# Optimization experiments

Hardware: AMD Instinct MI355X
Metric: run time of the kernel (lower is better)

Reference implementation:

```python
import jax, jax.numpy as jnp
import numpy as np

B, S, DIM = 4, 1024, 4096
HQ, HKV, HD = 32, 8, 128
MAX_SEQ = 2048
START_POS = 1024
THETA = 10000.0


def _rope_tables(start, seqlen, head_dim, theta):
    inv = 1.0 / (theta ** (np.arange(0, head_dim, 2, dtype=np.float32) / head_dim))
    pos = np.arange(start, start + seqlen, dtype=np.float32)
    ang = np.outer(pos, inv)  # [S, HD/2]
    return jnp.asarray(np.cos(ang)), jnp.asarray(np.sin(ang))


def setup_inputs() -> dict:
    key = jax.random.key(0)
    ks = jax.random.split(key, 8)
    sc = 1.0 / np.sqrt(DIM)
    x = jax.random.normal(ks[0], (B, S, DIM), jnp.float32)
    wq = jax.random.normal(ks[1], (DIM, HQ * HD), jnp.float32) * sc
    wk = jax.random.normal(ks[2], (DIM, HKV * HD), jnp.float32) * sc
    wv = jax.random.normal(ks[3], (DIM, HKV * HD), jnp.float32) * sc
    wo = jax.random.normal(ks[4], (HQ * HD, DIM), jnp.float32) * sc
    cache_k = jax.random.normal(ks[5], (B, MAX_SEQ, HKV, HD), jnp.float32)
    cache_v = jax.random.normal(ks[6], (B, MAX_SEQ, HKV, HD), jnp.float32)
    cos, sin = _rope_tables(START_POS, S, HD, THETA)
    return {"x": x, "wq": wq, "wk": wk, "wv": wv, "wo": wo,
            "freqs_cos": cos, "freqs_sin": sin,
            "cache_k": cache_k, "cache_v": cache_v, "start_pos": START_POS}


def _apply_rope(t, cos, sin):
    # t: [B, S, H, HD]; cos/sin: [S, HD/2]
    b, s, h, d = t.shape
    tr = t.reshape(b, s, h, d // 2, 2)
    xr, xi = tr[..., 0], tr[..., 1]
    c = cos[None, :, None, :]
    sn = sin[None, :, None, :]
    outr = xr * c - xi * sn
    outi = xr * sn + xi * c
    return jnp.stack([outr, outi], axis=-1).reshape(b, s, h, d)


def reference(x, wq, wk, wv, wo, freqs_cos, freqs_sin, cache_k, cache_v, start_pos):
    b, s, _ = x.shape
    rep = HQ // HKV
    q = (x @ wq).reshape(b, s, HQ, HD)
    k = (x @ wk).reshape(b, s, HKV, HD)
    v = (x @ wv).reshape(b, s, HKV, HD)
    q = _apply_rope(q, freqs_cos, freqs_sin)
    k = _apply_rope(k, freqs_cos, freqs_sin)
    # write new K/V into the cache at start_pos (static int -> static slice)
    cache_k = cache_k.at[:, start_pos:start_pos + s].set(k)
    cache_v = cache_v.at[:, start_pos:start_pos + s].set(v)
    keys = cache_k[:, : start_pos + s]     # [B, KV, HKV, HD]
    values = cache_v[:, : start_pos + s]
    # GQA: group query heads with their KV head instead of materializing repeat_kv
    qg = q.reshape(b, s, HKV, rep, HD)
    scores = jnp.einsum('bqhrd,bkhd->bhrqk', qg, keys) / jnp.sqrt(
        jnp.asarray(HD, x.dtype))
    probs = jax.nn.softmax(scores, axis=-1).astype(x.dtype)
    out = jnp.einsum('bhrqk,bkhd->bqhrd', probs, values)
    out = out.reshape(b, s, HQ * HD)
    return out @ wo
```

## Files before the change

### kernel.cpp

```cpp
#include <hip/hip_runtime.h>

typedef _Float16 half_t;
typedef _Float16 half8 __attribute__((ext_vector_type(8)));
typedef _Float16 half4v __attribute__((ext_vector_type(4)));
typedef _Float16 half2v __attribute__((ext_vector_type(2)));
typedef float floatx4 __attribute__((ext_vector_type(4)));

#define TOK 4096
#define DIM 4096
#define S_LEN 1024
#define B_SZ 4
#define HQ_N 32
#define HKV_N 8
#define HD_N 128
#define L_KV 2048
#define NKV 1024
#define NKV2 2048
#define QK_SCALE 0.08838834764831845f
#define LOG2E 1.4426950408889634f

__device__ __forceinline__ void gload_lds16(const void* g, void* l) {
  __builtin_amdgcn_global_load_lds(
      (const __attribute__((address_space(1))) unsigned int*)g,
      (__attribute__((address_space(3))) unsigned int*)l, 16, 0, 0);
}

__device__ __forceinline__ float max3f(float a, float b, float c) {
  return fmaxf(fmaxf(a, b), c);
}

__global__ __launch_bounds__(256) void prep_kernel(const float* __restrict__ x,
                                                   const float* __restrict__ wq,
                                                   const float* __restrict__ wk,
                                                   const float* __restrict__ wv,
                                                   const float* __restrict__ wo,
                                                   half_t* __restrict__ xh,
                                                   half_t* __restrict__ wqT,
                                                   half_t* __restrict__ kvT,
                                                   half_t* __restrict__ woT) {
  __shared__ half_t T[64 * 65];
  const int bid = blockIdx.x;
  const int tid = threadIdx.x;
  if (bid >= 10240) {
    int t = (bid - 10240) * 256 + tid;
    floatx4 v = *((const floatx4*)x + t);
    half4v o;
    o[0] = (half_t)v[0]; o[1] = (half_t)v[1]; o[2] = (half_t)v[2]; o[3] = (half_t)v[3];
    *((half4v*)xh + t) = o;
    return;
  }
  const float* in; half_t* out; int N; int lb;
  if (bid < 4096)      { in = wq; out = wqT; N = 4096; lb = bid; }
  else if (bid < 5120) { in = wk; out = kvT; N = 1024; lb = bid - 4096; }
  else if (bid < 6144) { in = wv; out = kvT + (size_t)NKV * DIM; N = 1024; lb = bid - 5120; }
  else                 { in = wo; out = woT; N = 4096; lb = bid - 6144; }
  const int nbx = N >> 6;
  const int n0 = (lb % nbx) * 64, k0 = (lb / nbx) * 64;
  #pragma unroll
  for (int i = 0; i < 16; ++i) {
    int idx = i * 256 + tid;
    int r = idx >> 6, c = idx & 63;
    T[c * 65 + r] = (half_t)in[(size_t)(k0 + r) * N + n0 + c];
  }
  __syncthreads();
  #pragma unroll
  for (int i = 0; i < 16; ++i) {
    int idx = i * 256 + tid;
    int rn = idx >> 6, ck = idx & 63;
    out[(size_t)(n0 + rn) * DIM + k0 + ck] = T[rn * 65 + ck];
  }
}

template <typename OT>
__global__ __launch_bounds__(256) void gemm_f16(const half_t* __restrict__ A,
                                                const half_t* __restrict__ BT,
                                                OT* __restrict__ C,
                                                int M, int N, int K) {
  __shared__ half_t As[128 * 32];
  __shared__ half_t Bs[128 * 32];
  const int tid = threadIdx.x;
  const int lane = tid & 63;
  const int w = tid >> 6;
  const int wr = w >> 1, wc = w & 1;
  const int g = lane >> 4, qr = lane & 15;
  const int m0 = blockIdx.y * 128, n0 = blockIdx.x * 128;
  floatx4 acc[4][4] = {};
  const int chb0 = tid & 192;
  for (int k0 = 0; k0 < K; k0 += 32) {
    #pragma unroll
    for (int i = 0; i < 2; ++i) {
      int chb = chb0 + 256 * i;
      int ch = chb + lane;
      int row = ch >> 2, c8 = ch & 3;
      gload_lds16(A + (size_t)(m0 + row) * K + k0 + c8 * 8, (char*)As + chb * 16);
      gload_lds16(BT + (size_t)(n0 + row) * K + k0 + c8 * 8, (char*)Bs + chb * 16);
    }
    __syncthreads();
    half8 af[4], bf[4];
    const int koff = g * 8;
    #pragma unroll
    for (int m = 0; m < 4; ++m)
      af[m] = *(const half8*)&As[(wr * 64 + m * 16 + qr) * 32 + koff];
    #pragma unroll
    for (int n = 0; n < 4; ++n)
      bf[n] = *(const half8*)&Bs[(wc * 64 + n * 16 + qr) * 32 + koff];
    #pragma unroll
    for (int m = 0; m < 4; ++m)
      #pragma unroll
      for (int n = 0; n < 4; ++n)
        acc[m][n] = __builtin_amdgcn_mfma_f32_16x16x32_f16(af[m], bf[n], acc[m][n], 0, 0, 0);
    __syncthreads();
  }
  #pragma unroll
  for (int m = 0; m < 4; ++m) {
    int rb = m0 + wr * 64 + m * 16 + g * 4;
    #pragma unroll
    for (int n = 0; n < 4; ++n) {
      int col = n0 + wc * 64 + n * 16 + qr;
      #pragma unroll
      for (int r = 0; r < 4; ++r)
        C[(size_t)(rb + r) * N + col] = (OT)acc[m][n][r];
    }
  }
}

template <typename OT, bool ROPE>
__global__ __launch_bounds__(512) void gemm256(const half_t* __restrict__ A,
                                               const half_t* __restrict__ BT,
                                               OT* __restrict__ C,
                                               const float* __restrict__ fc,
                                               const float* __restrict__ fs,
                                               half_t* __restrict__ qh,
                                               int M, int N, int K) {
  __shared__ __align__(16) char smem[131072];
  const int tid = threadIdx.x;
  const int lane = tid & 63, w = tid >> 6;
  const int g = lane >> 4, qr = lane & 15;
  const int wm = w >> 2, wn = w & 3;
  const int nbx = N >> 8;
  const int nwg = gridDim.x;
  const int cpx = nwg >> 3;
  const int bid = ((int)blockIdx.x & 7) * cpx + ((int)blockIdx.x >> 3);
  const int bx = bid % nbx, by = bid / nbx;
  const int m0 = by << 8, n0 = bx << 8;
  const int NT = K >> 6;

  const int ch0 = tid, ch1 = tid + 512;
  const int sr0 = ch0 >> 3, sc0 = (ch0 & 7) ^ (sr0 & 7);
  const int sr1 = ch1 >> 3, sc1 = (ch1 & 7) ^ (sr1 & 7);
  const size_t so0 = (size_t)sr0 * K + sc0 * 8;
  const size_t so1 = (size_t)sr1 * K + sc1 * 8;
  const int wb = (w * 64) * 16;
  const half_t* Ab = A + (size_t)m0 * K;
  const half_t* Bb = BT + (size_t)n0 * K;

#define G_STAGE(gsrc, ldst)                                   \
  do {                                                        \
    gload_lds16((gsrc) + so0, (char*)(ldst) + wb);            \
    gload_lds16((gsrc) + so1, (char*)(ldst) + wb + 8192);     \
  } while (0)

#define FRAG(base, row, kb) \
  (*(const half8*)((base) + ((((row) * 128) + (kb)) ^ (((row) & 7) << 4))))

  G_STAGE(Ab, smem);
  G_STAGE(Ab + (size_t)128 * K, smem + 16384);
  G_STAGE(Bb, smem + 65536);
  G_STAGE(Bb + (size_t)128 * K, smem + 81920);
  G_STAGE(Ab + 64, smem + 32768);
  G_STAGE(Bb + 64, smem + 98304);
  asm volatile("s_waitcnt vmcnt(4)" ::: "memory");
  __builtin_amdgcn_s_barrier();

  floatx4 acc[8][4] = {};
  half8 aF[4][2], bF0[2][2], bF1[2][2];

#define MFMA_Q(mh, nh, BF)                                                     \
  do {                                                                         \
    __builtin_amdgcn_s_setprio(1);                                             \
    _Pragma("unroll") for (int mf = 0; mf < 4; ++mf)                           \
    _Pragma("unroll") for (int nf = 0; nf < 2; ++nf)                           \
    _Pragma("unroll") for (int kk = 0; kk < 2; ++kk)                           \
      acc[(mh)*4 + mf][(nh)*2 + nf] = __builtin_amdgcn_mfma_f32_16x16x32_f16(  \
          aF[mf][kk], BF[nf][kk], acc[(mh)*4 + mf][(nh)*2 + nf], 0, 0, 0);     \
    __builtin_amdgcn_s_setprio(0);                                             \
  } while (0)

  for (int t = 0; t < NT; ++t) {
    const char* Ac = smem + ((t & 1) ? 32768 : 0);
    const char* Bc = smem + 65536 + ((t & 1) ? 32768 : 0);
    char* An = smem + ((t & 1) ? 0 : 32768);
    char* Bn = smem + 65536 + ((t & 1) ? 0 : 32768);
    const int t1 = (t + 1 < NT) ? t + 1 : NT - 1;
    const int t2 = (t + 2 < NT) ? t + 2 : NT - 1;
    #pragma unroll
    for (int mf = 0; mf < 4; ++mf)
      #pragma unroll
      for (int kk = 0; kk < 2; ++kk)
        aF[mf][kk] = FRAG(Ac, wm * 128 + mf * 16 + qr, kk * 64 + g * 16);
    #pragma unroll
    for (int nf = 0; nf < 2; ++nf)
      #pragma unroll
      for (int kk = 0; kk < 2; ++kk)
        bF0[nf][kk] = FRAG(Bc, wn * 64 + nf * 16 + qr, kk * 64 + g * 16);
    G_STAGE(Ab + (size_t)128 * K + t1 * 64, An + 16384);
    __builtin_amdgcn_s_barrier();
    asm volatile("s_waitcnt lgkmcnt(0)" ::: "memory");
    MFMA_Q(0, 0, bF0);
    __builtin_amdgcn_s_barrier();
    #pragma unroll
    for (int nf = 0; nf < 2; ++nf)
      #pragma unroll
      for (int kk = 0; kk < 2; ++kk)
        bF1[nf][kk] = FRAG(Bc, wn * 64 + 32 + nf * 16 + qr, kk * 64 + g * 16);
    G_STAGE(Bb + (size_t)128 * K + t1 * 64, Bn + 16384);
    __builtin_amdgcn_s_barrier();
    asm volatile("s_waitcnt lgkmcnt(0)" ::: "memory");
    MFMA_Q(0, 1, bF1);
    __builtin_amdgcn_s_barrier();
    #pragma unroll
    for (int mf = 0; mf < 4; ++mf)
      #pragma unroll
      for (int kk = 0; kk < 2; ++kk)
        aF[mf][kk] = FRAG(Ac, wm * 128 + 64 + mf * 16 + qr, kk * 64 + g * 16);
    __builtin_amdgcn_s_barrier();
    asm volatile("s_waitcnt lgkmcnt(0)" ::: "memory");
    MFMA_Q(1, 1, bF1);
    __builtin_amdgcn_s_barrier();
    G_STAGE(Ab + (size_t)t2 * 64, (char*)Ac);
    G_STAGE(Bb + (size_t)t2 * 64, (char*)Bc);
    __builtin_amdgcn_s_barrier();
    MFMA_Q(1, 0, bF0);
    asm volatile("s_waitcnt vmcnt(4)" ::: "memory");
    __builtin_amdgcn_s_barrier();
  }
  #pragma unroll
  for (int mh = 0; mh < 2; ++mh)
    #pragma unroll
    for (int mf = 0; mf < 4; ++mf) {
      const int rb = m0 + wm * 128 + mh * 64 + mf * 16 + g * 4;
      #pragma unroll
      for (int nh = 0; nh < 2; ++nh)
        #pragma unroll
        for (int nf = 0; nf < 2; ++nf) {
          const int col = n0 + wn * 64 + nh * 32 + nf * 16 + qr;
          floatx4 v = acc[mh * 4 + mf][nh * 2 + nf];
          if constexpr (ROPE) {
            const float QS2 = QK_SCALE * LOG2E;
            const int d = col & 127, hqh = col >> 7, j = d >> 1;
            #pragma unroll
            for (int r = 0; r < 4; ++r) {
              float pv = __shfl_xor(v[r], 1, 64);
              const int tokr = rb + r;
              const int s = tokr & 1023, bb = tokr >> 10;
              float c = fc[s * 64 + j], sn = fs[s * 64 + j];
              float outv = (qr & 1) ? (v[r] * c + pv * sn) : (v[r] * c - pv * sn);
              qh[(((size_t)(bb * HQ_N + hqh)) * S_LEN + s) * HD_N + d] =
                  (half_t)(outv * QS2);
            }
          } else {
            #pragma unroll
            for (int r = 0; r < 4; ++r)
              C[(size_t)(rb + r) * N + col] = (OT)v[r];
          }
        }
    }
#undef G_STAGE
#undef FRAG
#undef MFMA_Q
}

__global__ __launch_bounds__(256) void pack_k_kernel(const half_t* __restrict__ kvf,
                                                     const float* __restrict__ cache_k,
                                                     const float* __restrict__ cosT,
                                                     const float* __restrict__ sinT,
                                                     half_t* __restrict__ kh) {
  int t = blockIdx.x * 256 + threadIdx.x;
  int j = t & 63;
  int h = (t >> 6) & 7;
  int pos = (t >> 9) & 2047;
  int b = t >> 20;
  float xr, xi;
  if (pos < 1024) {
    const float* src = cache_k + ((size_t)(b * L_KV + pos) * HKV_N + h) * HD_N + 2 * j;
    xr = src[0]; xi = src[1];
  } else {
    int s = pos - 1024;
    const half_t* src = kvf + (size_t)(b * S_LEN + s) * NKV2 + h * HD_N + 2 * j;
    float r0 = (float)src[0], i0 = (float)src[1];
    float c = cosT[s * 64 + j], sn = sinT[s * 64 + j];
    xr = r0 * c - i0 * sn;
    xi = r0 * sn + i0 * c;
  }
  half2v o; o[0] = (half_t)xr; o[1] = (half_t)xi;
  *(half2v*)(kh + ((size_t)(b * HKV_N + h) * L_KV + pos) * HD_N + 2 * j) = o;
}

__global__ __launch_bounds__(256) void pack_vt_kernel(const half_t* __restrict__ kvf,
                                                      const float* __restrict__ cache_v,
                                                      half_t* __restrict__ vt) {
  __shared__ half_t T[128 * 129];
  const int tid = threadIdx.x;
  const int blk = blockIdx.x;
  const int pt = blk & 15;
  const int h = (blk >> 4) & 7;
  const int b = blk >> 7;
  const int p0 = pt * 128;
  #pragma unroll
  for (int i = 0; i < 64; ++i) {
    int idx = i * 256 + tid;
    int p = idx >> 7, d = idx & 127;
    int pos = p0 + p;
    float v;
    if (pos < 1024)
      v = cache_v[((size_t)(b * L_KV + pos) * HKV_N + h) * HD_N + d];
    else
      v = (float)kvf[(size_t)(b * S_LEN + (pos - 1024)) * NKV2 + NKV + h * HD_N + d];
    T[d * 129 + p] = (half_t)v;
  }
  __syncthreads();
  #pragma unroll
  for (int i = 0; i < 64; ++i) {
    int idx = i * 256 + tid;
    int d = idx >> 7, p = idx & 127;
    vt[((size_t)(b * HKV_N + h) * HD_N + d) * L_KV + p0 + p] = T[d * 129 + p];
  }
}

__global__ __launch_bounds__(256, 2) void attn_kernel(const half_t* __restrict__ qh,
                                                      const half_t* __restrict__ kh,
                                                      const half_t* __restrict__ vt,
                                                      half_t* __restrict__ ah) {
  __shared__ __align__(16) char smem[73728];
  const int tid = threadIdx.x;
  const int lane = tid & 63, w = tid >> 6;
  const int g = lane >> 4, qr = lane & 15;
  const int hq = blockIdx.x, qt = blockIdx.y, b = blockIdx.z;
  const int hkv = hq >> 2;
  const half_t* qbase =
      qh + ((size_t)((b * HQ_N + hq) * S_LEN) + qt * 128 + w * 16 + qr) * HD_N;
  half8 qfA[4], qfB[4];
  #pragma unroll
  for (int c = 0; c < 4; ++c) {
    qfA[c] = *(const half8*)(qbase + g * 8 + c * 32);
    qfB[c] = *(const half8*)(qbase + (size_t)64 * HD_N + g * 8 + c * 32);
  }
  floatx4 accA[8] = {}, accB[8] = {};
  float mA = -1e30f, lA = 0.f, mB = -1e30f, lB = 0.f;
  const half_t* kg = kh + (size_t)(b * HKV_N + hkv) * L_KV * HD_N;
  const half_t* vg = vt + (size_t)(b * HKV_N + hkv) * HD_N * L_KV;

  const int sw = (qr & 7) << 4;
  const char* kqkP[4];
  #pragma unroll
  for (int c = 0; c < 4; ++c) kqkP[c] = smem + qr * 256 + ((g * 16 + c * 64) ^ sw);
  const char* vP[2];
  #pragma unroll
  for (int kc = 0; kc < 2; ++kc)
    vP[kc] = smem + 32768 + qr * 128 + ((kc * 64 + g * 16) ^ sw);
  char* pB = smem + 65536 + w * 2048 + qr * 128;
  char* pwQ[4];
  #pragma unroll
  for (int ts = 0; ts < 4; ++ts) pwQ[ts] = pB + ((ts * 32 + g * 8) ^ sw);
  const char* prR[2];
  #pragma unroll
  for (int kc = 0; kc < 2; ++kc) prR[kc] = pB + ((kc * 64 + g * 16) ^ sw);

  const int r0 = tid >> 4;
  const int c8k = (tid & 15) ^ (r0 & 7);
  const half_t* kp[4];
  #pragma unroll
  for (int j = 0; j < 4; ++j) kp[j] = kg + (size_t)(r0 + 16 * j) * HD_N + c8k * 8;
  const int d0v = tid >> 3;
  const int p8v = (tid & 7) ^ (d0v & 7);
  const half_t* vp[4];
  #pragma unroll
  for (int j = 0; j < 4; ++j) vp[j] = vg + (size_t)(d0v + 32 * j) * L_KV + p8v * 8;
  const int ldsb = (tid & 192) * 16;

#define ISSUE_STAGE(NKB)                                                     \
  do {                                                                       \
    _Pragma("unroll") for (int j2 = 0; j2 < 4; ++j2)                         \
      gload_lds16(kp[j2], smem + (NKB) + ldsb + j2 * 4096);                  \
    _Pragma("unroll") for (int j2 = 0; j2 < 4; ++j2)                         \
      gload_lds16(vp[j2], smem + 32768 + (NKB) + ldsb + j2 * 4096);          \
    _Pragma("unroll") for (int j2 = 0; j2 < 4; ++j2) {                       \
      kp[j2] += 8192; vp[j2] += 64;                                          \
    }                                                                        \
  } while (0)

#define QKT2(KB)                                                               \
  do {                                                                         \
    __builtin_amdgcn_s_setprio(1);                                             \
    _Pragma("unroll") for (int ts = 0; ts < 4; ++ts) {                         \
      floatx4 tqA = {0.f, 0.f, 0.f, 0.f}, tqB = {0.f, 0.f, 0.f, 0.f};          \
      _Pragma("unroll") for (int c = 0; c < 4; ++c) {                          \
        half8 kfr = *(const half8*)(kqkP[c] + (KB) + ts * 4096);               \
        tqA = __builtin_amdgcn_mfma_f32_16x16x32_f16(kfr, qfA[c], tqA, 0,0,0); \
        tqB = __builtin_amdgcn_mfma_f32_16x16x32_f16(kfr, qfB[c], tqB, 0,0,0); \
      }                                                                        \
      scA[ts*4+0]=tqA[0]; scA[ts*4+1]=tqA[1];                                  \
      scA[ts*4+2]=tqA[2]; scA[ts*4+3]=tqA[3];                                  \
      scB[ts*4+0]=tqB[0]; scB[ts*4+1]=tqB[1];                                  \
      scB[ts*4+2]=tqB[2]; scB[ts*4+3]=tqB[3];                                  \
    }                                                                          \
    __builtin_amdgcn_s_setprio(0);                                             \
  } while (0)

#define SOFTMAX(SC, ACC, MR, LR, PF)                                           \
  do {                                                                         \
    float pmax = fmaxf(                                                        \
        max3f(max3f(SC[0], SC[1], SC[2]), max3f(SC[3], SC[4], SC[5]),          \
              max3f(SC[6], SC[7], SC[8])),                                     \
        max3f(max3f(SC[9], SC[10], SC[11]), max3f(SC[12], SC[13], SC[14]),     \
              SC[15]));                                                        \
    pmax = fmaxf(pmax, __shfl_xor(pmax, 16, 64));                              \
    pmax = fmaxf(pmax, __shfl_xor(pmax, 32, 64));                              \
    const bool skip = __all(pmax - MR <= 8.f);                                 \
    const float mnew = skip ? MR : fmaxf(MR, pmax);                            \
    float rs = 0.f;                                                            \
    _Pragma("unroll") for (int j = 0; j < 16; ++j) {                           \
      float p;                                                                 \
      asm("v_exp_f32 %0, %1" : "=v"(p) : "v"(SC[j] - mnew));                   \
      SC[j] = p; rs += p;                                                      \
    }                                                                          \
    rs += __shfl_xor(rs, 16, 64);                                              \
    rs += __shfl_xor(rs, 32, 64);                                              \
    if (skip) {                                                                \
      LR += rs;                                                                \
    } else {                                                                   \
      float scl;                                                               \
      asm("v_exp_f32 %0, %1" : "=v"(scl) : "v"(MR - mnew));                    \
      LR = LR * scl + rs;                                                      \
      float f0 = __shfl(scl, g * 4 + 0, 64), f1 = __shfl(scl, g * 4 + 1, 64);  \
      float f2 = __shfl(scl, g * 4 + 2, 64), f3 = __shfl(scl, g * 4 + 3, 64);  \
      _Pragma("unroll") for (int n = 0; n < 8; ++n) {                          \
        ACC[n][0] *= f0; ACC[n][1] *= f1; ACC[n][2] *= f2; ACC[n][3] *= f3;    \
      }                                                                        \
      MR = mnew;                                                               \
    }                                                                          \
    _Pragma("unroll") for (int ts = 0; ts < 4; ++ts) {                         \
      half2v lo = __builtin_bit_cast(                                          \
          half2v, __builtin_amdgcn_cvt_pkrtz(SC[ts * 4 + 0], SC[ts * 4 + 1])); \
      half2v hi = __builtin_bit_cast(                                          \
          half2v, __builtin_amdgcn_cvt_pkrtz(SC[ts * 4 + 2], SC[ts * 4 + 3])); \
      *(half4v*)(pwQ[ts]) = __builtin_shufflevector(lo, hi, 0, 1, 2, 3);       \
    }                                                                          \
    PF[0] = *(const half8*)(prR[0]);                                           \
    PF[1] = *(const half8*)(prR[1]);                                           \
  } while (0)

#define PV2(KB)                                                                \
  do {                                                                         \
    __builtin_amdgcn_s_setprio(1);                                             \
    _Pragma("unroll") for (int kc = 0; kc < 2; ++kc)                           \
      _Pragma("unroll") for (int n = 0; n < 8; ++n) {                          \
        half8 vfr = *(const half8*)(vP[kc] + (KB) + n * 2048);                 \
        accA[n] = __builtin_amdgcn_mfma_f32_16x16x32_f16(pfA[kc], vfr,         \
                                                         accA[n], 0, 0, 0);   \
        accB[n] = __builtin_amdgcn_mfma_f32_16x16x32_f16(pfB[kc], vfr,         \
                                                         accB[n], 0, 0, 0);   \
      }                                                                        \
    __builtin_amdgcn_s_setprio(0);                                             \
  } while (0)

#define COMPUTE2(KB)                          \
  do {                                        \
    float scA[16], scB[16];                   \
    half8 pfA[2], pfB[2];                     \
    QKT2(KB);                                 \
    SOFTMAX(scA, accA, mA, lA, pfA);          \
    SOFTMAX(scB, accB, mB, lB, pfB);          \
    PV2(KB);                                  \
  } while (0)

#define ENDBAR                                          \
  do {                                                  \
    asm volatile("s_waitcnt vmcnt(0)" ::: "memory");    \
    __builtin_amdgcn_s_barrier();                       \
  } while (0)

  ISSUE_STAGE(0);
  ENDBAR;
  for (int it = 0; it < 15; ++it) {
    ISSUE_STAGE(16384); COMPUTE2(0);     ENDBAR;
    ISSUE_STAGE(0);     COMPUTE2(16384); ENDBAR;
  }
  ISSUE_STAGE(16384); COMPUTE2(0); ENDBAR;
  COMPUTE2(16384);

#define WRITE_OUT(ACC, LR, SOFF)                                            \
  do {                                                                      \
    float il0 = 1.f / __shfl(LR, g * 4 + 0, 64);                            \
    float il1 = 1.f / __shfl(LR, g * 4 + 1, 64);                            \
    float il2 = 1.f / __shfl(LR, g * 4 + 2, 64);                            \
    float il3 = 1.f / __shfl(LR, g * 4 + 3, 64);                            \
    const int tokb = b * S_LEN + qt * 128 + (SOFF) + w * 16 + g * 4;        \
    _Pragma("unroll") for (int n = 0; n < 8; ++n) {                         \
      const int col = hq * HD_N + n * 16 + qr;                              \
      ah[(size_t)(tokb + 0) * DIM + col] = (half_t)(ACC[n][0] * il0);       \
      ah[(size_t)(tokb + 1) * DIM + col] = (half_t)(ACC[n][1] * il1);       \
      ah[(size_t)(tokb + 2) * DIM + col] = (half_t)(ACC[n][2] * il2);       \
      ah[(size_t)(tokb + 3) * DIM + col] = (half_t)(ACC[n][3] * il3);       \
    }                                                                       \
  } while (0)

  WRITE_OUT(accA, lA, 0);
  WRITE_OUT(accB, lB, 64);
#undef ISSUE_STAGE
#undef QKT2
#undef SOFTMAX
#undef PV2
#undef COMPUTE2
#undef ENDBAR
#undef WRITE_OUT
}

extern "C" void kernel_launch(void* const* d_in, const int* in_sizes, int n_in,
                              void* d_out, int out_size, void* d_ws, size_t ws_size,
                              hipStream_t stream) {
  (void)in_sizes; (void)n_in; (void)out_size; (void)ws_size;
  const float* x = (const float*)d_in[0];
  const float* wq = (const float*)d_in[1];
  const float* wk = (const float*)d_in[2];
  const float* wv = (const float*)d_in[3];
  const float* wo = (const float*)d_in[4];
  const float* fc = (const float*)d_in[5];
  const float* fs = (const float*)d_in[6];
  const float* ck = (const float*)d_in[7];
  const float* cv = (const float*)d_in[8];

  char* ws = (char*)d_ws;
  size_t off = 0;
  auto alloc = [&](size_t bytes) {
    char* p = ws + off;
    off += (bytes + 255) & ~(size_t)255;
    return p;
  };
  half_t* xh    = (half_t*)alloc((size_t)TOK * DIM * 2);
  half_t* wqT   = (half_t*)alloc((size_t)DIM * DIM * 2);
  half_t* kvT   = (half_t*)alloc((size_t)NKV2 * DIM * 2);
  half_t* woT   = (half_t*)alloc((size_t)DIM * DIM * 2);
  half_t* qh    = (half_t*)alloc((size_t)B_SZ * HQ_N * S_LEN * HD_N * 2);
  half_t* kvf16 = (half_t*)alloc((size_t)TOK * NKV2 * 2);
  half_t* kh    = (half_t*)alloc((size_t)B_SZ * HKV_N * L_KV * HD_N * 2);
  half_t* vth   = (half_t*)alloc((size_t)B_SZ * HKV_N * HD_N * L_KV * 2);
  half_t* ah    = wqT;

  prep_kernel<<<dim3(26624), dim3(256), 0, stream>>>(x, wq, wk, wv, wo, xh, wqT, kvT, woT);
  gemm256<half_t, true><<<dim3((TOK / 256) * (DIM / 256)), dim3(512), 0, stream>>>(
      xh, wqT, (half_t*)nullptr, fc, fs, qh, TOK, DIM, DIM);
  gemm_f16<half_t><<<dim3(NKV2 / 128, TOK / 128), dim3(256), 0, stream>>>(xh, kvT, kvf16, TOK, NKV2, DIM);
  pack_k_kernel<<<dim3(B_SZ * L_KV * HKV_N * 64 / 256), dim3(256), 0, stream>>>(kvf16, ck, fc, fs, kh);
  pack_vt_kernel<<<dim3(B_SZ * HKV_N * (L_KV / 128)), dim3(256), 0, stream>>>(kvf16, cv, vth);
  attn_kernel<<<dim3(HQ_N, S_LEN / 128, B_SZ), dim3(256), 0, stream>>>(qh, kh, vth, ah);
  gemm256<float, false><<<dim3((TOK / 256) * (DIM / 256)), dim3(512), 0, stream>>>(
      ah, woT, (float*)d_out, nullptr, nullptr, nullptr, TOK, DIM, DIM);
}
```

Measured before the change: 626.4 us.

## Single-buffer K/V tiles in attention to fit four blocks per CU

Replaces the double-buffered K/V LDS staging with single K and V buffers and interleaves their loads with the softmax and PV phases, cutting shared memory from 72KB to 40KB. Launch bounds rise to four blocks per CU so that more waves hide latency. In exchange each iteration has more barriers, prefetch distance is shorter, and the tighter register budget may cause spills.

```diff
diff --git a/kernel.cpp b/kernel.cpp
--- a/kernel.cpp
+++ b/kernel.cpp
@@ -327,11 +327,11 @@
   }
 }
 
-__global__ __launch_bounds__(256, 2) void attn_kernel(const half_t* __restrict__ qh,
+__global__ __launch_bounds__(256, 4) void attn_kernel(const half_t* __restrict__ qh,
                                                       const half_t* __restrict__ kh,
                                                       const half_t* __restrict__ vt,
                                                       half_t* __restrict__ ah) {
-  __shared__ __align__(16) char smem[73728];
+  __shared__ __align__(16) char smem[40960];
   const int tid = threadIdx.x;
   const int lane = tid & 63, w = tid >> 6;
   const int g = lane >> 4, qr = lane & 15;
@@ -357,8 +357,8 @@
   const char* vP[2];
   #pragma unroll
   for (int kc = 0; kc < 2; ++kc)
-    vP[kc] = smem + 32768 + qr * 128 + ((kc * 64 + g * 16) ^ sw);
-  char* pB = smem + 65536 + w * 2048 + qr * 128;
+    vP[kc] = smem + 16384 + qr * 128 + ((kc * 64 + g * 16) ^ sw);
+  char* pB = smem + 32768 + w * 2048 + qr * 128;
   char* pwQ[4];
   #pragma unroll
   for (int ts = 0; ts < 4; ++ts) pwQ[ts] = pB + ((ts * 32 + g * 8) ^ sw);
@@ -378,24 +378,29 @@
   for (int j = 0; j < 4; ++j) vp[j] = vg + (size_t)(d0v + 32 * j) * L_KV + p8v * 8;
   const int ldsb = (tid & 192) * 16;
 
-#define ISSUE_STAGE(NKB)                                                     \
+#define STAGE_K                                                              \
   do {                                                                       \
-    _Pragma("unroll") for (int j2 = 0; j2 < 4; ++j2)                         \
-      gload_lds16(kp[j2], smem + (NKB) + ldsb + j2 * 4096);                  \
-    _Pragma("unroll") for (int j2 = 0; j2 < 4; ++j2)                         \
-      gload_lds16(vp[j2], smem + 32768 + (NKB) + ldsb + j2 * 4096);          \
     _Pragma("unroll") for (int j2 = 0; j2 < 4; ++j2) {                       \
-      kp[j2] += 8192; vp[j2] += 64;                                          \
+      gload_lds16(kp[j2], smem + ldsb + j2 * 4096);                          \
+      kp[j2] += 8192;                                                        \
     }                                                                        \
   } while (0)
 
-#define QKT2(KB)                                                               \
+#define STAGE_V                                                              \
+  do {                                                                       \
+    _Pragma("unroll") for (int j2 = 0; j2 < 4; ++j2) {                       \
+      gload_lds16(vp[j2], smem + 16384 + ldsb + j2 * 4096);                  \
+      vp[j2] += 64;                                                          \
+    }                                                                        \
+  } while (0)
+
+#define QKT2                                                                   \
   do {                                                                         \
     __builtin_amdgcn_s_setprio(1);                                             \
     _Pragma("unroll") for (int ts = 0; ts < 4; ++ts) {                         \
       floatx4 tqA = {0.f, 0.f, 0.f, 0.f}, tqB = {0.f, 0.f, 0.f, 0.f};          \
       _Pragma("unroll") for (int c = 0; c < 4; ++c) {                          \
-        half8 kfr = *(const half8*)(kqkP[c] + (KB) + ts * 4096);               \
+        half8 kfr = *(const half8*)(kqkP[c] + ts * 4096);                      \
         tqA = __builtin_amdgcn_mfma_f32_16x16x32_f16(kfr, qfA[c], tqA, 0,0,0); \
         tqB = __builtin_amdgcn_mfma_f32_16x16x32_f16(kfr, qfB[c], tqB, 0,0,0); \
       }                                                                        \
@@ -450,12 +455,12 @@
     PF[1] = *(const half8*)(prR[1]);                                           \
   } while (0)
 
-#define PV2(KB)                                                                \
+#define PV2                                                                    \
   do {                                                                         \
     __builtin_amdgcn_s_setprio(1);                                             \
     _Pragma("unroll") for (int kc = 0; kc < 2; ++kc)                           \
       _Pragma("unroll") for (int n = 0; n < 8; ++n) {                          \
-        half8 vfr = *(const half8*)(vP[kc] + (KB) + n * 2048);                 \
+        half8 vfr = *(const half8*)(vP[kc] + n * 2048);                        \
         accA[n] = __builtin_amdgcn_mfma_f32_16x16x32_f16(pfA[kc], vfr,         \
                                                          accA[n], 0, 0, 0);   \
         accB[n] = __builtin_amdgcn_mfma_f32_16x16x32_f16(pfB[kc], vfr,         \
@@ -464,30 +469,34 @@
     __builtin_amdgcn_s_setprio(0);                                             \
   } while (0)
 
-#define COMPUTE2(KB)                          \
-  do {                                        \
-    float scA[16], scB[16];                   \
-    half8 pfA[2], pfB[2];                     \
-    QKT2(KB);                                 \
-    SOFTMAX(scA, accA, mA, lA, pfA);          \
-    SOFTMAX(scB, accB, mB, lB, pfB);          \
-    PV2(KB);                                  \
-  } while (0)
-
-#define ENDBAR                                          \
-  do {                                                  \
-    asm volatile("s_waitcnt vmcnt(0)" ::: "memory");    \
-    __builtin_amdgcn_s_barrier();                       \
-  } while (0)
-
-  ISSUE_STAGE(0);
-  ENDBAR;
-  for (int it = 0; it < 15; ++it) {
-    ISSUE_STAGE(16384); COMPUTE2(0);     ENDBAR;
-    ISSUE_STAGE(0);     COMPUTE2(16384); ENDBAR;
-  }
-  ISSUE_STAGE(16384); COMPUTE2(0); ENDBAR;
-  COMPUTE2(16384);
+#define BAR __builtin_amdgcn_s_barrier()
+#define WAITV(N) asm volatile("s_waitcnt vmcnt(" #N ")" ::: "memory")
+
+  STAGE_K; STAGE_V;
+  WAITV(0); BAR;
+  for (int kt = 0; kt < 31; ++kt) {
+    float scA[16], scB[16];
+    half8 pfA[2], pfB[2];
+    QKT2;
+    BAR;
+    STAGE_K;
+    SOFTMAX(scA, accA, mA, lA, pfA);
+    SOFTMAX(scB, accB, mB, lB, pfB);
+    WAITV(4); BAR;
+    PV2;
+    BAR;
+    STAGE_V;
+    WAITV(4); BAR;
+  }
+  {
+    float scA[16], scB[16];
+    half8 pfA[2], pfB[2];
+    QKT2;
+    SOFTMAX(scA, accA, mA, lA, pfA);
+    SOFTMAX(scB, accB, mB, lB, pfB);
+    WAITV(0); BAR;
+    PV2;
+  }
 
 #define WRITE_OUT(ACC, LR, SOFF)                                            \
   do {                                                                      \
@@ -507,12 +516,13 @@
 
   WRITE_OUT(accA, lA, 0);
   WRITE_OUT(accB, lB, 64);
-#undef ISSUE_STAGE
+#undef STAGE_K
+#undef STAGE_V
 #undef QKT2
 #undef SOFTMAX
 #undef PV2
-#undef COMPUTE2
-#undef ENDBAR
+#undef BAR
+#undef WAITV
 #undef WRITE_OUT
 }
 
```

Measured after the change: 940.8 us. 50.2% more time.
